# Kernel optimization log

Hardware: AMD Instinct MI355X
Metric: run time of the kernel (lower is better)

The kernel has to match this reference:

```python
import jax, jax.numpy as jnp
import numpy as np

B, L, D, NUM_ITEM, NBIN, LAYER_NUM = 1000, 50, 128, 100000, 10, 3


def _gru(x, W_ih, W_hh, b_ih, b_hh):
    # x: [B, L, Din]; torch gate order r,z,n; returns (outputs [B,L,H], h_last [B,H])
    bsz = x.shape[0]
    H = W_hh.shape[1]
    xp = jnp.einsum('bld,gd->blg', x, W_ih) + b_ih  # [B, L, 3H]

    def step(h, xp_t):
        gh = h @ W_hh.T + b_hh
        xr, xz, xn = jnp.split(xp_t, 3, axis=-1)
        hr, hz, hn = jnp.split(gh, 3, axis=-1)
        r = jax.nn.sigmoid(xr + hr)
        z = jax.nn.sigmoid(xz + hz)
        n = jnp.tanh(xn + r * hn)
        h_new = (1.0 - z) * n + z * h
        return h_new, h_new

    h0 = jnp.zeros((bsz, H), x.dtype)
    h_last, outs = jax.lax.scan(step, h0, jnp.swapaxes(xp, 0, 1))
    return jnp.swapaxes(outs, 0, 1), h_last


def _t_gcn(h, edge, edge_weight, layer_num):
    # edge-list weighted propagation; average of all layer outputs (LightGCN-style)
    src, dst = edge[0], edge[1]
    acc = h
    x = h
    for _ in range(layer_num):
        msg = x[src] * edge_weight[:, None]
        x = jax.ops.segment_sum(msg, dst, num_segments=h.shape[0])
        acc = acc + x
    return acc / (layer_num + 1)


def setup_inputs() -> dict:
    rng = np.random.default_rng(0)
    sess_len = (np.arange(B) % L) + 1
    T = int(sess_len.sum())
    seg_ids = np.repeat(np.arange(B), sess_len)
    pos_ids = np.concatenate([np.arange(L - l, L) for l in sess_len])
    n_nodes, n_edges = T, 2 * T

    key = jax.random.key(0)
    ks = jax.random.split(key, 24)
    std = 0.1

    def p(k, shape):
        return (jax.random.normal(k, shape, jnp.float32) * std)

    inp = {
        'items': jnp.asarray(rng.integers(0, NUM_ITEM, n_nodes), jnp.int32),
        'edge': jnp.asarray(rng.integers(0, n_nodes, (2, n_edges)), jnp.int32),
        'edge_weight': jax.random.uniform(ks[0], (n_edges,), jnp.float32),
        'item2idx': jnp.arange(T, dtype=jnp.int32),
        'bins': jnp.asarray(rng.integers(0, NBIN, (B, L)), jnp.int32),
        'seg_ids': jnp.asarray(seg_ids, jnp.int32),
        'pos_ids': jnp.asarray(pos_ids, jnp.int32),
        'sess_len': jnp.asarray(sess_len, jnp.int32),
        'item_emb': p(ks[1], (NUM_ITEM, D)),
        'bin_emb': p(ks[2], (NBIN, D)),
        'Wih_f': p(ks[3], (3 * D, D)), 'Whh_f': p(ks[4], (3 * D, D)),
        'bih_f': p(ks[5], (3 * D,)), 'bhh_f': p(ks[6], (3 * D,)),
        'Wih_b': p(ks[7], (3 * D, D)), 'Whh_b': p(ks[8], (3 * D, D)),
        'bih_b': p(ks[9], (3 * D,)), 'bhh_b': p(ks[10], (3 * D,)),
        'w1': p(ks[11], (1, 2 * D)),
        'w2': p(ks[12], (D, 2 * D)),
        'v3': p(ks[13], (1, D)),
        'Wih_s': p(ks[14], (3 * D, D)), 'Whh_s': p(ks[15], (3 * D, D)),
        'bih_s': p(ks[16], (3 * D,)), 'bhh_s': p(ks[17], (3 * D,)),
        'w3': p(ks[18], (1, D)), 'b3': p(ks[19], (1,)),
    }
    return inp


def reference(items, edge, edge_weight, item2idx, bins, seg_ids, pos_ids, sess_len,
              item_emb, bin_emb,
              Wih_f, Whh_f, bih_f, bhh_f, Wih_b, Whh_b, bih_b, bhh_b,
              w1, w2, v3, Wih_s, Whh_s, bih_s, bhh_s, w3, b3):
    # graph propagation over unique items, gathered back to session tokens
    h = item_emb[items]                                  # [N, D]
    h_final = _t_gcn(h, edge, edge_weight, LAYER_NUM)[item2idx]  # [T, D]

    # time-bin embedding + bidirectional GRU (dropout = identity in eval)
    e = bin_emb[bins]                                    # [B, L, D]
    out_f, _ = _gru(e, Wih_f, Whh_f, bih_f, bhh_f)
    out_b, _ = _gru(e[:, ::-1], Wih_b, Whh_b, bih_b, bhh_b)
    e_dir = jnp.concatenate([out_f, out_b[:, ::-1]], axis=-1)  # [B, L, 2D]

    b_gate = jax.nn.sigmoid(e_dir @ w1.T)                # [B, L, 1]
    e_hat_full = b_gate * e_dir[:, :, :D] + (1.0 - b_gate) * e_dir[:, :, D:]
    # take last sess_len[i] steps of each session -> ragged gather
    e_hat = e_hat_full[seg_ids, pos_ids]                 # [T, D]

    beta = jnp.tanh(jnp.concatenate([h_final, e_hat], axis=-1) @ w2.T) @ v3.T  # [T, 1]
    c = beta * h_final                                   # [T, D]

    z_long = jax.ops.segment_sum(c, seg_ids, num_segments=B)  # [B, D]

    # right-aligned pad then short GRU, keep final hidden
    c_pad = jnp.zeros((B, L, D), c.dtype).at[seg_ids, pos_ids].set(c)
    _, z_short = _gru(c_pad, Wih_s, Whh_s, bih_s, bhh_s)  # [B, D]

    f = jax.nn.sigmoid((z_long + z_short) @ w3.T + b3)   # [B, 1]
    z_final = f * z_long + (1.0 - f) * z_short
    return z_final @ item_emb.T                          # [B, NUM_ITEM]
```

## Files before the change

### kernel.cpp

```cpp
#include <hip/hip_runtime.h>
#include <hip/hip_fp16.h>

#define D    128
#define L    50
#define G3   384
#define NBIN 10
#define NNMAX 25600

#define FBM 128
#define FBN 128

typedef float f32x4 __attribute__((ext_vector_type(4)));
typedef short s16x8 __attribute__((ext_vector_type(8)));

#define MFMA_B16(a,b,c) __builtin_amdgcn_mfma_f32_16x16x32_bf16(a,b,c,0,0,0)

__device__ __forceinline__ float sigm(float x){ return 1.f/(1.f+__expf(-x)); }
__device__ __forceinline__ float tanh_fast(float x){
  float xx = fminf(fmaxf(x,-15.f),15.f);
  float e  = __expf(2.f*xx);
  return (e-1.f)/(e+1.f);
}

#define SPLIT1(x, hu, lu) { unsigned u_ = __float_as_uint(x); hu = u_ >> 16; \
  float hf_ = __uint_as_float(u_ & 0xffff0000u); float lf_ = (x) - hf_; \
  lu = __float_as_uint(lf_) >> 16; }

__device__ __forceinline__ void split8(f32x4 a, f32x4 b, s16x8& hi, s16x8& lo){
  s16x8 h, l;
#pragma unroll
  for (int i=0;i<4;++i){
    unsigned hu, lu;
    SPLIT1(a[i], hu, lu)
    h[i] = (short)hu; l[i] = (short)lu;
  }
#pragma unroll
  for (int i=0;i<4;++i){
    unsigned hu, lu;
    SPLIT1(b[i], hu, lu)
    h[4+i] = (short)hu; l[4+i] = (short)lu;
  }
  hi = h; lo = l;
}

__global__ void k_prep(const float* __restrict__ bin_emb,
                       const float* __restrict__ Wf, const float* __restrict__ bf,
                       const float* __restrict__ Wb, const float* __restrict__ bb,
                       const float* __restrict__ item_emb, const int* __restrict__ items,
                       float* __restrict__ tabf, float* __restrict__ tabb,
                       float* __restrict__ accA, float* __restrict__ xB,
                       float* __restrict__ cpad, int* __restrict__ tokmap,
                       unsigned short* __restrict__ zhi, unsigned short* __restrict__ zlo,
                       long long NG, long long BLD, int BL){
  const long long r1 = 7680, r2 = r1 + NG, r3 = r2 + BLD, r4 = r3 + BL;
  const long long ZP = 1024*128;
  const long long total = r4 + 2*ZP;
  for (long long i = (long long)blockIdx.x*256 + threadIdx.x; i < total;
       i += (long long)gridDim.x*256){
    if (i < r1){
      int id = (int)i; int dirr = id / (NBIN*G3); int rr = id % (NBIN*G3);
      int v = rr / G3, g = rr % G3;
      const float* W  = dirr ? Wb : Wf;
      const float* bi = dirr ? bb : bf;
      float a = bi[g];
      for (int d = 0; d < D; ++d) a += bin_emb[v*D+d]*W[g*D+d];
      (dirr ? tabb : tabf)[v*G3+g] = a;
    } else if (i < r2){
      long long k = i - r1;
      int nn = (int)(k>>7), d = (int)(k&127);
      float v = item_emb[(size_t)items[nn]*D + d];
      accA[k] = v; xB[k] = v;
    } else if (i < r3){
      cpad[i - r2] = 0.f;
    } else if (i < r4){
      tokmap[i - r3] = -1;
    } else {
      long long k = i - r4;
      if (k < ZP) zhi[k] = 0;
      else        zlo[k - ZP] = 0;
    }
  }
}

__global__ __launch_bounds__(1024) void k_csr1(const int* __restrict__ dst,
                                               int* __restrict__ off, int* __restrict__ cursor,
                                               int nn, int ne){
  __shared__ int degs[NNMAX];
  __shared__ int part[1024];
  int tid = threadIdx.x;
  for (int i = tid; i < nn; i += 1024) degs[i] = 0;
  __syncthreads();
  for (int e = tid; e < ne; e += 1024) atomicAdd(&degs[dst[e]], 1);
  __syncthreads();
  int chunk = (nn + 1023) >> 10;
  int c0 = tid*chunk;
  int s = 0;
  for (int k = 0; k < chunk; ++k){ int v = c0+k; if (v < nn) s += degs[v]; }
  part[tid] = s; __syncthreads();
  for (int d = 1; d < 1024; d <<= 1){
    int v = (tid >= d) ? part[tid-d] : 0;
    __syncthreads();
    part[tid] += v;
    __syncthreads();
  }
  int run = part[tid] - s;
  for (int k = 0; k < chunk; ++k){
    int v = c0+k;
    if (v < nn){ off[v] = run; cursor[v] = run; run += degs[v]; }
  }
  if (tid == 1023) off[nn] = part[1023];
}
__global__ void k_fill(const int* __restrict__ src, const int* __restrict__ dst,
                       const float* __restrict__ ew, int* __restrict__ cursor,
                       int* __restrict__ csrs, float* __restrict__ csrw, int ne){
  int e = blockIdx.x*256 + threadIdx.x;
  if (e >= ne) return;
  int p = atomicAdd(&cursor[dst[e]], 1);
  csrs[p] = src[e];
  csrw[p] = ew[e];
}
__global__ void k_gath(const float* __restrict__ x, float* __restrict__ xn,
                       float* __restrict__ acc,
                       const int* __restrict__ off, const int* __restrict__ csrs,
                       const float* __restrict__ csrw, int n){
  int i = blockIdx.x*256 + threadIdx.x;
  if (i >= n) return;
  int v = i >> 7, d = i & (D-1);
  int a = off[v], b = off[v+1];
  float s = 0.f;
  for (int k = a; k < b; ++k)
    s += x[(size_t)csrs[k]*D + d] * csrw[k];
  xn[i] = s;
  acc[i] += s;
}

__global__ __launch_bounds__(512) void k_gru_fb(
    const float* __restrict__ Whh_f, const float* __restrict__ Whh_b,
    const float* __restrict__ bhh_f, const float* __restrict__ bhh_b,
    const float* __restrict__ tabf,  const float* __restrict__ tabb,
    const int*   __restrict__ bins,  int Bn,
    float* __restrict__ outf, float* __restrict__ outbrev){
  const int dir = blockIdx.y;
  const int b0  = blockIdx.x * 16;
  const float* Whh = dir ? Whh_b : Whh_f;
  const float* bhh = dir ? bhh_b : bhh_f;
  const float* tab = dir ? tabb  : tabf;
  float* outp = dir ? outbrev : outf;

  __shared__ unsigned short hhi[2*16*128];
  __shared__ unsigned short hlo[2*16*128];
  __shared__ float xts[NBIN*G3];
  __shared__ int   binr[16][L];

  const int tid = threadIdx.x;
  const int wv = tid>>6, lane = tid&63;
  const int l15 = lane&15, lk = lane>>4;
  const int jb = wv*16;
  const int jq = jb + lk*4;

  s16x8 whi[3][4], wlo[3][4];
#pragma unroll
  for (int g3i = 0; g3i < 3; ++g3i)
#pragma unroll
    for (int ks = 0; ks < 4; ++ks){
      const f32x4* s = (const f32x4*)&Whh[(size_t)(g3i*D + jb + l15)*D + ks*32 + lk*8];
      split8(s[0], s[1], whi[g3i][ks], wlo[g3i][ks]);
    }
  f32x4 bhv[3];
#pragma unroll
  for (int g3i = 0; g3i < 3; ++g3i) bhv[g3i] = *(const f32x4*)&bhh[g3i*D + jq];

  for (int i = tid; i < NBIN*G3; i += 512) xts[i] = tab[i];
  for (int i = tid; i < 16*L; i += 512){
    int r = i / L, t = i % L;
    binr[r][t] = (b0 + r < Bn) ? bins[(b0+r)*L + (dir ? (L-1-t) : t)] : 0;
  }
  for (int i = tid; i < 2*16*128; i += 512){ hhi[i] = 0; hlo[i] = 0; }

  const int sess = l15;
  const bool sv = (b0 + sess) < Bn;
  float hreg[4] = {0.f,0.f,0.f,0.f};
  const int wbyte = sess*256 + (((jq>>3) ^ (sess&7))<<4) + ((jq&7)<<1);
  int cur = 0;
  __syncthreads();

  for (int t = 0; t < L; ++t){
    f32x4 c0a={0.f,0.f,0.f,0.f}, c1a=c0a, c2a=c0a, c0b=c0a, c1b=c0a, c2b=c0a;
    const int rb = cur*4096;
#pragma unroll
    for (int ks = 0; ks < 2; ++ks){
      int off = rb + l15*256 + ((((ks<<2)+lk) ^ (l15&7)) << 4);
      s16x8 bh8 = *(const s16x8*)((const char*)hhi + off);
      s16x8 bl8 = *(const s16x8*)((const char*)hlo + off);
      c0a = MFMA_B16(whi[0][ks], bh8, c0a); c0a = MFMA_B16(whi[0][ks], bl8, c0a); c0a = MFMA_B16(wlo[0][ks], bh8, c0a);
      c1a = MFMA_B16(whi[1][ks], bh8, c1a); c1a = MFMA_B16(whi[1][ks], bl8, c1a); c1a = MFMA_B16(wlo[1][ks], bh8, c1a);
      c2a = MFMA_B16(whi[2][ks], bh8, c2a); c2a = MFMA_B16(whi[2][ks], bl8, c2a); c2a = MFMA_B16(wlo[2][ks], bh8, c2a);
    }
#pragma unroll
    for (int ks = 2; ks < 4; ++ks){
      int off = rb + l15*256 + ((((ks<<2)+lk) ^ (l15&7)) << 4);
      s16x8 bh8 = *(const s16x8*)((const char*)hhi + off);
      s16x8 bl8 = *(const s16x8*)((const char*)hlo + off);
      c0b = MFMA_B16(whi[0][ks], bh8, c0b); c0b = MFMA_B16(whi[0][ks], bl8, c0b); c0b = MFMA_B16(wlo[0][ks], bh8, c0b);
      c1b = MFMA_B16(whi[1][ks], bh8, c1b); c1b = MFMA_B16(whi[1][ks], bl8, c1b); c1b = MFMA_B16(wlo[1][ks], bh8, c1b);
      c2b = MFMA_B16(whi[2][ks], bh8, c2b); c2b = MFMA_B16(whi[2][ks], bl8, c2b); c2b = MFMA_B16(wlo[2][ks], bh8, c2b);
    }
    f32x4 c0 = c0a + c0b, c1 = c1a + c1b, c2 = c2a + c2b;
    int bin = binr[sess][t];
    const float* xb = &xts[bin*G3];
    f32x4 xr4 = *(const f32x4*)&xb[jq];
    f32x4 xz4 = *(const f32x4*)&xb[D + jq];
    f32x4 xn4 = *(const f32x4*)&xb[2*D + jq];
    ushort4 hi4, lo4;
    f32x4 hn4;
#pragma unroll
    for (int qq = 0; qq < 4; ++qq){
      float gr = c0[qq] + bhv[0][qq];
      float gz = c1[qq] + bhv[1][qq];
      float gn = c2[qq] + bhv[2][qq];
      float rr = sigm(xr4[qq] + gr);
      float zz = sigm(xz4[qq] + gz);
      float nn = tanh_fast(xn4[qq] + rr*gn);
      float hnew = (1.f-zz)*nn + zz*hreg[qq];
      hreg[qq] = hnew;
      unsigned hu, lu; SPLIT1(hnew, hu, lu)
      ((unsigned short*)&hi4)[qq] = (unsigned short)hu;
      ((unsigned short*)&lo4)[qq] = (unsigned short)lu;
      hn4[qq] = hnew;
    }
    int wb = (cur^1)*4096 + wbyte;
    *(ushort4*)((char*)hhi + wb) = hi4;
    *(ushort4*)((char*)hlo + wb) = lo4;
    if (sv){
      float4 o = make_float4(hn4[0],hn4[1],hn4[2],hn4[3]);
      *(float4*)&outp[((size_t)(b0+sess)*L + (dir ? (L-1-t) : t))*D + jq] = o;
    }
    __syncthreads();
    cur ^= 1;
  }
}

__global__ __launch_bounds__(512) void k_beta2(
    const float* __restrict__ outf, const float* __restrict__ outbrev,
    const float* __restrict__ accA, const int* __restrict__ idxmap,
    const float* __restrict__ w1, const float* __restrict__ w2,
    const float* __restrict__ v3,
    const int* __restrict__ seg, const int* __restrict__ pos, int T,
    float* __restrict__ c_pad, int* __restrict__ tokmap){
  __shared__ unsigned short Bhi[32*256];
  __shared__ unsigned short Blo[32*256];
  __shared__ float w1s[2*D];
  __shared__ float betas[32];

  const int tid = threadIdx.x;
  const int wv = tid>>6, lane = tid&63;
  const int l15 = lane&15, lk = lane>>4;

  s16x8 w2hi[8], w2lo[8];
#pragma unroll
  for (int ks = 0; ks < 8; ++ks){
    const f32x4* s = (const f32x4*)&w2[(size_t)(wv*16 + l15)*256 + ks*32 + lk*8];
    split8(s[0], s[1], w2hi[ks], w2lo[ks]);
  }
  f32x4 v3q = *(const f32x4*)&v3[wv*16 + lk*4];
  for (int i = tid; i < 2*D; i += 512) w1s[i] = w1[i];
  __syncthreads();

  const int tok = tid >> 4;
  const int d0  = (tid & 15) * 8;
  const int sw  = (tid & 15) ^ (tok & 7);
  const int ntiles = (T + 31) >> 5;

  for (int tile = blockIdx.x; tile < ntiles; tile += gridDim.x){
    int t = tile*32 + tok;
    bool valid = (t < T);
    int sp = 0;
    f32x4 ef0 = {0,0,0,0}, ef1 = ef0, eb0 = ef0, eb1 = ef0, hf0 = ef0, hf1 = ef0;
    if (valid){
      sp = seg[t]*L + pos[t];
      const f32x4* pf = (const f32x4*)&outf[(size_t)sp*D + d0];
      const f32x4* pb = (const f32x4*)&outbrev[(size_t)sp*D + d0];
      const f32x4* ph = (const f32x4*)&accA[(size_t)idxmap[t]*D + d0];
      ef0 = pf[0]; ef1 = pf[1];
      eb0 = pb[0]; eb1 = pb[1];
      hf0 = ph[0]; hf1 = ph[1];
#pragma unroll
      for (int k=0;k<4;++k){ hf0[k]*=0.25f; hf1[k]*=0.25f; }
    }
    float p = 0.f;
#pragma unroll
    for (int k=0;k<4;++k){
      p += ef0[k]*w1s[d0+k]     + eb0[k]*w1s[D+d0+k];
      p += ef1[k]*w1s[d0+4+k]   + eb1[k]*w1s[D+d0+4+k];
    }
    p += __shfl_xor(p,1); p += __shfl_xor(p,2);
    p += __shfl_xor(p,4); p += __shfl_xor(p,8);
    float gate = sigm(p);
    f32x4 eh0, eh1;
#pragma unroll
    for (int k=0;k<4;++k){
      eh0[k] = gate*ef0[k] + (1.f-gate)*eb0[k];
      eh1[k] = gate*ef1[k] + (1.f-gate)*eb1[k];
    }
    {
      s16x8 h8, l8;
      split8(hf0, hf1, h8, l8);
      int byte = tok*512 + (sw<<4);
      *(s16x8*)((char*)Bhi + byte) = h8;
      *(s16x8*)((char*)Blo + byte) = l8;
      split8(eh0, eh1, h8, l8);
      byte = tok*512 + ((16+((tid&15)^(tok&7)))<<4);
      *(s16x8*)((char*)Bhi + byte) = h8;
      *(s16x8*)((char*)Blo + byte) = l8;
    }
    if (tid < 32) betas[tid] = 0.f;
    __syncthreads();
#pragma unroll
    for (int tt = 0; tt < 2; ++tt){
      f32x4 ca = {0.f,0.f,0.f,0.f}, cb = ca;
#pragma unroll
      for (int ks = 0; ks < 4; ++ks){
        int s_ = ((ks<<2)+lk);
        int off = (tt*16 + l15)*512 + ((s_ ^ (l15&7)) << 4);
        s16x8 bh8 = *(const s16x8*)((const char*)Bhi + off);
        s16x8 bl8 = *(const s16x8*)((const char*)Blo + off);
        ca = MFMA_B16(w2hi[ks], bh8, ca);
        ca = MFMA_B16(w2hi[ks], bl8, ca);
        ca = MFMA_B16(w2lo[ks], bh8, ca);
      }
#pragma unroll
      for (int ks = 4; ks < 8; ++ks){
        int s_ = ((ks<<2)+lk);
        int off = (tt*16 + l15)*512 + ((s_ ^ (l15&7)) << 4);
        s16x8 bh8 = *(const s16x8*)((const char*)Bhi + off);
        s16x8 bl8 = *(const s16x8*)((const char*)Blo + off);
        cb = MFMA_B16(w2hi[ks], bh8, cb);
        cb = MFMA_B16(w2hi[ks], bl8, cb);
        cb = MFMA_B16(w2lo[ks], bh8, cb);
      }
      f32x4 c = ca + cb;
      float pv = 0.f;
#pragma unroll
      for (int qq = 0; qq < 4; ++qq) pv += tanh_fast(c[qq]) * v3q[qq];
      pv += __shfl_xor(pv, 16);
      pv += __shfl_xor(pv, 32);
      if (lk == 0) atomicAdd(&betas[tt*16 + l15], pv);
    }
    __syncthreads();
    if (valid){
      float beta = betas[tok];
      f32x4 c0, c1;
#pragma unroll
      for (int k=0;k<4;++k){ c0[k] = beta*hf0[k]; c1[k] = beta*hf1[k]; }
      f32x4* pc = (f32x4*)&c_pad[(size_t)sp*D + d0];
      pc[0] = c0; pc[1] = c1;
      if ((tid & 15) == 0) tokmap[sp] = t;
    }
    __syncthreads();
  }
}

__global__ __launch_bounds__(512) void k_xps2(
    const float* __restrict__ c_pad, const int* __restrict__ seg,
    const int* __restrict__ pos, const float* __restrict__ Wih,
    const float* __restrict__ bih, int T, float* __restrict__ xps,
    float* __restrict__ zl, int Bn){
  __shared__ unsigned short Bhi[32*128];
  __shared__ unsigned short Blo[32*128];
  __shared__ float us[32*388];
  __shared__ float bihs[G3];

  const int tid = threadIdx.x;
  const int wv = tid>>6, lane = tid&63;
  const int l15 = lane&15, lk = lane>>4;
  const int gbase = wv * 48;

  for (int i = blockIdx.x*512 + tid; i < Bn*D; i += gridDim.x*512){
    int b = i >> 7, j = i & (D-1);
    float s = 0.f;
    for (int l = 0; l < L; ++l) s += c_pad[((size_t)b*L + l)*D + j];
    zl[i] = s;
  }

  s16x8 whi[3][4], wlo[3][4];
#pragma unroll
  for (int mt = 0; mt < 3; ++mt)
#pragma unroll
    for (int ks = 0; ks < 4; ++ks){
      const f32x4* s = (const f32x4*)&Wih[(size_t)(gbase + mt*16 + l15)*D + ks*32 + lk*8];
      split8(s[0], s[1], whi[mt][ks], wlo[mt][ks]);
    }
  for (int i = tid; i < G3; i += 512) bihs[i] = bih[i];
  __syncthreads();

  const int tok = tid >> 4;
  const int d0  = (tid & 15) * 8;
  const int ntiles = (T + 31) >> 5;

  for (int tile = blockIdx.x; tile < ntiles; tile += gridDim.x){
    int t = tile*32 + tok;
    bool valid = (t < T);
    f32x4 x0 = {0,0,0,0}, x1 = x0;
    if (valid){
      int sp = seg[t]*L + pos[t];
      const f32x4* pc = (const f32x4*)&c_pad[(size_t)sp*D + d0];
      x0 = pc[0]; x1 = pc[1];
    }
    {
      s16x8 h8, l8;
      split8(x0, x1, h8, l8);
      int byte = tok*256 + ((((tid&15)) ^ (tok&7))<<4);
      *(s16x8*)((char*)Bhi + byte) = h8;
      *(s16x8*)((char*)Blo + byte) = l8;
    }
    __syncthreads();
#pragma unroll
    for (int tt = 0; tt < 2; ++tt){
      f32x4 ca[3], cb[3];
#pragma unroll
      for (int mt = 0; mt < 3; ++mt){ f32x4 z = {0,0,0,0}; ca[mt] = z; cb[mt] = z; }
#pragma unroll
      for (int ks = 0; ks < 2; ++ks){
        int off = (tt*16 + l15)*256 + ((((ks<<2)+lk) ^ (l15&7)) << 4);
        s16x8 bh8 = *(const s16x8*)((const char*)Bhi + off);
        s16x8 bl8 = *(const s16x8*)((const char*)Blo + off);
        ca[0] = MFMA_B16(whi[0][ks], bh8, ca[0]); ca[0] = MFMA_B16(whi[0][ks], bl8, ca[0]); ca[0] = MFMA_B16(wlo[0][ks], bh8, ca[0]);
        ca[1] = MFMA_B16(whi[1][ks], bh8, ca[1]); ca[1] = MFMA_B16(whi[1][ks], bl8, ca[1]); ca[1] = MFMA_B16(wlo[1][ks], bh8, ca[1]);
        ca[2] = MFMA_B16(whi[2][ks], bh8, ca[2]); ca[2] = MFMA_B16(whi[2][ks], bl8, ca[2]); ca[2] = MFMA_B16(wlo[2][ks], bh8, ca[2]);
      }
#pragma unroll
      for (int ks = 2; ks < 4; ++ks){
        int off = (tt*16 + l15)*256 + ((((ks<<2)+lk) ^ (l15&7)) << 4);
        s16x8 bh8 = *(const s16x8*)((const char*)Bhi + off);
        s16x8 bl8 = *(const s16x8*)((const char*)Blo + off);
        cb[0] = MFMA_B16(whi[0][ks], bh8, cb[0]); cb[0] = MFMA_B16(whi[0][ks], bl8, cb[0]); cb[0] = MFMA_B16(wlo[0][ks], bh8, cb[0]);
        cb[1] = MFMA_B16(whi[1][ks], bh8, cb[1]); cb[1] = MFMA_B16(whi[1][ks], bl8, cb[1]); cb[1] = MFMA_B16(wlo[1][ks], bh8, cb[1]);
        cb[2] = MFMA_B16(whi[2][ks], bh8, cb[2]); cb[2] = MFMA_B16(whi[2][ks], bl8, cb[2]); cb[2] = MFMA_B16(wlo[2][ks], bh8, cb[2]);
      }
#pragma unroll
      for (int mt = 0; mt < 3; ++mt){
        f32x4 c = ca[mt] + cb[mt];
        *(f32x4*)&us[(tt*16 + l15)*388 + gbase + mt*16 + lk*4] = c;
      }
    }
    __syncthreads();
    for (int i4 = tid; i4 < 32*96; i4 += 512){
      int tk = i4 / 96, g4 = (i4 % 96) * 4;
      int tt2 = tile*32 + tk;
      if (tt2 < T){
        f32x4 u4 = *(const f32x4*)&us[tk*388 + g4];
        f32x4 b4 = *(const f32x4*)&bihs[g4];
#pragma unroll
        for (int k=0;k<4;++k) u4[k] += b4[k];
        *(f32x4*)&xps[(size_t)tt2*G3 + g4] = u4;
      }
    }
    __syncthreads();
  }
}

__global__ __launch_bounds__(512) void k_grus(
    const float* __restrict__ Whh, const float* __restrict__ bhh,
    const float* __restrict__ bih,
    const float* __restrict__ xps, const int* __restrict__ tokmap,
    const float* __restrict__ zl, const float* __restrict__ w3,
    const float* __restrict__ b3, int Bn,
    unsigned short* __restrict__ zhi, unsigned short* __restrict__ zlo,
    const float* __restrict__ emb,
    unsigned short* __restrict__ ehp, unsigned short* __restrict__ elp,
    int NI, int nslots, int nGru){
  if (blockIdx.x >= nGru){
    int nb = gridDim.x - nGru;
    for (int s = (blockIdx.x - nGru)*512 + threadIdx.x; s < nslots; s += nb*512){
      int lane = s & 63;
      int nfw  = (s>>6) & 7;
      int kk   = (s>>9) & 3;
      int ntl  = s >> 11;
      int row  = ntl*128 + (nfw>>2)*64 + (nfw&3)*16 + (lane&15);
      int d0   = kk*32 + (lane>>4)*8;
      s16x8 h8 = {0,0,0,0,0,0,0,0}, l8 = h8;
      if (row < NI){
        const f32x4* src = (const f32x4*)&emb[(size_t)row*D + d0];
        split8(src[0], src[1], h8, l8);
      }
      *(s16x8*)&ehp[(size_t)s*8] = h8;
      *(s16x8*)&elp[(size_t)s*8] = l8;
    }
    return;
  }
  const int b0 = blockIdx.x * 16;

  __shared__ unsigned short hhi[2*16*128];
  __shared__ unsigned short hlo[2*16*128];
  __shared__ int   maprow[16][L];
  __shared__ float redg[16];

  const int tid = threadIdx.x;
  const int wv = tid>>6, lane = tid&63;
  const int l15 = lane&15, lk = lane>>4;
  const int jb = wv*16;
  const int jq = jb + lk*4;

  s16x8 whi[3][4], wlo[3][4];
#pragma unroll
  for (int g3i = 0; g3i < 3; ++g3i)
#pragma unroll
    for (int ks = 0; ks < 4; ++ks){
      const f32x4* s = (const f32x4*)&Whh[(size_t)(g3i*D + jb + l15)*D + ks*32 + lk*8];
      split8(s[0], s[1], whi[g3i][ks], wlo[g3i][ks]);
    }
  f32x4 bhv[3], biv[3];
#pragma unroll
  for (int g3i = 0; g3i < 3; ++g3i){
    bhv[g3i] = *(const f32x4*)&bhh[g3i*D + jq];
    biv[g3i] = *(const f32x4*)&bih[g3i*D + jq];
  }
  for (int i = tid; i < 16*L; i += 512){
    int r = i / L, t = i % L;
    maprow[r][t] = (b0 + r < Bn) ? tokmap[(b0+r)*L + t] : -1;
  }
  for (int i = tid; i < 2*16*128; i += 512){ hhi[i] = 0; hlo[i] = 0; }

  const int sess = l15;
  const bool sv = (b0 + sess) < Bn;
  float hreg[4] = {0.f,0.f,0.f,0.f};
  const int wbyte = sess*256 + (((jq>>3) ^ (sess&7))<<4) + ((jq&7)<<1);
  int cur = 0;
  __syncthreads();

  for (int t = 0; t < L; ++t){
    int tok = maprow[sess][t];
    f32x4 xr4, xz4, xn4;
    if (tok >= 0){
      const float* xb = &xps[(size_t)tok*G3];
      xr4 = *(const f32x4*)&xb[jq];
      xz4 = *(const f32x4*)&xb[D + jq];
      xn4 = *(const f32x4*)&xb[2*D + jq];
    } else { xr4 = biv[0]; xz4 = biv[1]; xn4 = biv[2]; }
    f32x4 c0a={0.f,0.f,0.f,0.f}, c1a=c0a, c2a=c0a, c0b=c0a, c1b=c0a, c2b=c0a;
    const int rb = cur*4096;
#pragma unroll
    for (int ks = 0; ks < 2; ++ks){
      int off = rb + l15*256 + ((((ks<<2)+lk) ^ (l15&7)) << 4);
      s16x8 bh8 = *(const s16x8*)((const char*)hhi + off);
      s16x8 bl8 = *(const s16x8*)((const char*)hlo + off);
      c0a = MFMA_B16(whi[0][ks], bh8, c0a); c0a = MFMA_B16(whi[0][ks], bl8, c0a); c0a = MFMA_B16(wlo[0][ks], bh8, c0a);
      c1a = MFMA_B16(whi[1][ks], bh8, c1a); c1a = MFMA_B16(whi[1][ks], bl8, c1a); c1a = MFMA_B16(wlo[1][ks], bh8, c1a);
      c2a = MFMA_B16(whi[2][ks], bh8, c2a); c2a = MFMA_B16(whi[2][ks], bl8, c2a); c2a = MFMA_B16(wlo[2][ks], bh8, c2a);
    }
#pragma unroll
    for (int ks = 2; ks < 4; ++ks){
      int off = rb + l15*256 + ((((ks<<2)+lk) ^ (l15&7)) << 4);
      s16x8 bh8 = *(const s16x8*)((const char*)hhi + off);
      s16x8 bl8 = *(const s16x8*)((const char*)hlo + off);
      c0b = MFMA_B16(whi[0][ks], bh8, c0b); c0b = MFMA_B16(whi[0][ks], bl8, c0b); c0b = MFMA_B16(wlo[0][ks], bh8, c0b);
      c1b = MFMA_B16(whi[1][ks], bh8, c1b); c1b = MFMA_B16(whi[1][ks], bl8, c1b); c1b = MFMA_B16(wlo[1][ks], bh8, c1b);
      c2b = MFMA_B16(whi[2][ks], bh8, c2b); c2b = MFMA_B16(whi[2][ks], bl8, c2b); c2b = MFMA_B16(wlo[2][ks], bh8, c2b);
    }
    f32x4 c0 = c0a + c0b, c1 = c1a + c1b, c2 = c2a + c2b;
    ushort4 hi4, lo4;
#pragma unroll
    for (int qq = 0; qq < 4; ++qq){
      float gr = c0[qq] + bhv[0][qq];
      float gz = c1[qq] + bhv[1][qq];
      float gn = c2[qq] + bhv[2][qq];
      float rr = sigm(xr4[qq] + gr);
      float zz = sigm(xz4[qq] + gz);
      float nn = tanh_fast(xn4[qq] + rr*gn);
      float hnew = (1.f-zz)*nn + zz*hreg[qq];
      hreg[qq] = hnew;
      unsigned hu, lu; SPLIT1(hnew, hu, lu)
      ((unsigned short*)&hi4)[qq] = (unsigned short)hu;
      ((unsigned short*)&lo4)[qq] = (unsigned short)lu;
    }
    int wb = (cur^1)*4096 + wbyte;
    *(ushort4*)((char*)hhi + wb) = hi4;
    *(ushort4*)((char*)hlo + wb) = lo4;
    __syncthreads();
    cur ^= 1;
  }

  if (tid < 16) redg[tid] = 0.f;
  __syncthreads();
  f32x4 zl4 = {0.f,0.f,0.f,0.f};
  if (sv) zl4 = *(const f32x4*)&zl[(size_t)(b0+sess)*D + jq];
  f32x4 w34 = *(const f32x4*)&w3[jq];
  float part = 0.f;
#pragma unroll
  for (int qq = 0; qq < 4; ++qq) part += (zl4[qq] + hreg[qq]) * w34[qq];
  if (sv) atomicAdd(&redg[sess], part);
  __syncthreads();
  if (sv){
    float f = sigm(redg[sess] + b3[0]);
    ushort4 h4, l4;
#pragma unroll
    for (int qq = 0; qq < 4; ++qq){
      float zv = f*zl4[qq] + (1.f-f)*hreg[qq];
      unsigned hu, lu; SPLIT1(zv, hu, lu)
      ((unsigned short*)&h4)[qq] = (unsigned short)hu;
      ((unsigned short*)&l4)[qq] = (unsigned short)lu;
    }
    int row = b0 + sess;
    int mtile = row >> 7, r128 = row & 127;
    int wmr = r128 >> 6, mfr = (r128 >> 4) & 3, l15r = r128 & 15;
    int kkr = jq >> 5, lkr = (jq & 31) >> 3, e0 = jq & 7;
    int laner = lkr*16 + l15r;
    size_t slot = ((size_t)(((mtile*4 + kkr)*2 + wmr)*4 + mfr))*64 + laner;
    *(ushort4*)&zhi[slot*8 + e0] = h4;
    *(ushort4*)&zlo[slot*8 + e0] = l4;
  }
}

__global__ __launch_bounds__(256, 3) void k_fmm(
    const unsigned short* __restrict__ zhi, const unsigned short* __restrict__ zlo,
    const unsigned short* __restrict__ ehp, const unsigned short* __restrict__ elp,
    float* __restrict__ out, int NI, int Bsz){
  __shared__ float fs[64*136];

  int nwg = gridDim.x;
  int hw  = blockIdx.x;
  int q8 = nwg >> 3, r8 = nwg & 7;
  int xcd = hw & 7, idx = hw >> 3;
  int logical = (xcd < r8 ? xcd*(q8+1) : r8*(q8+1) + (xcd-r8)*q8) + idx;
  int ntile = logical >> 3;
  int mtile = logical & 7;
  int m0 = mtile*FBM;
  int n0 = ntile*FBN;

  const int t    = threadIdx.x;
  const int lane = t & 63;
  const int wid  = t >> 6;
  const int wm   = wid >> 1, wn = wid & 1;
  const int l15  = lane & 15, lk = lane >> 4;

  f32x4 acc[4][4];
#pragma unroll
  for (int i = 0; i < 4; ++i)
#pragma unroll
    for (int jj = 0; jj < 4; ++jj){ f32x4 z4 = {0.f,0.f,0.f,0.f}; acc[i][jj] = z4; }

#pragma unroll
  for (int kk = 0; kk < 4; ++kk){
    s16x8 ah[4], al[4], bh8[4], bl8[4];
#pragma unroll
    for (int mf = 0; mf < 4; ++mf){
      size_t slot = ((size_t)(((mtile*4 + kk)*2 + wm)*4 + mf))*64 + lane;
      ah[mf] = *(const s16x8*)&zhi[slot*8];
      al[mf] = *(const s16x8*)&zlo[slot*8];
    }
#pragma unroll
    for (int nf = 0; nf < 4; ++nf){
      size_t slot = ((size_t)((ntile*4 + kk)*8 + wn*4 + nf))*64 + lane;
      bh8[nf] = *(const s16x8*)&ehp[slot*8];
      bl8[nf] = *(const s16x8*)&elp[slot*8];
    }
#pragma unroll
    for (int mf = 0; mf < 4; ++mf)
#pragma unroll
      for (int nf = 0; nf < 4; ++nf){
        acc[mf][nf] = MFMA_B16(ah[mf], bh8[nf], acc[mf][nf]);
        acc[mf][nf] = MFMA_B16(ah[mf], bl8[nf], acc[mf][nf]);
        acc[mf][nf] = MFMA_B16(al[mf], bh8[nf], acc[mf][nf]);
      }
  }

#pragma unroll
  for (int p = 0; p < 2; ++p){
    __syncthreads();
    if (wm == p){
#pragma unroll
      for (int mf = 0; mf < 4; ++mf)
#pragma unroll
        for (int nf = 0; nf < 4; ++nf)
#pragma unroll
          for (int qq = 0; qq < 4; ++qq)
            fs[(mf*16 + lk*4 + qq)*136 + wn*64 + nf*16 + l15] = acc[mf][nf][qq];
    }
    __syncthreads();
#pragma unroll
    for (int it = 0; it < 8; ++it){
      int row = (t>>5) + it*8;
      int col = (t&31)*4;
      f32x4 v = *(const f32x4*)&fs[row*136 + col];
      int gr = m0 + p*64 + row;
      if (gr < Bsz && n0 + col < NI)
        __builtin_nontemporal_store(v, (f32x4*)&out[(size_t)gr*NI + n0 + col]);
    }
  }
}

extern "C" void kernel_launch(void* const* d_in, const int* in_sizes, int n_in,
                              void* d_out, int out_size, void* d_ws, size_t ws_size,
                              hipStream_t stream){
  const int*   items    = (const int*)d_in[0];
  const int*   edge     = (const int*)d_in[1];
  const float* ew       = (const float*)d_in[2];
  const int*   item2idx = (const int*)d_in[3];
  const int*   bins     = (const int*)d_in[4];
  const int*   seg      = (const int*)d_in[5];
  const int*   pos      = (const int*)d_in[6];
  const float* item_emb = (const float*)d_in[8];
  const float* bin_emb  = (const float*)d_in[9];
  const float* Wih_f = (const float*)d_in[10];
  const float* Whh_f = (const float*)d_in[11];
  const float* bih_f = (const float*)d_in[12];
  const float* bhh_f = (const float*)d_in[13];
  const float* Wih_b = (const float*)d_in[14];
  const float* Whh_b = (const float*)d_in[15];
  const float* bih_b = (const float*)d_in[16];
  const float* bhh_b = (const float*)d_in[17];
  const float* w1    = (const float*)d_in[18];
  const float* w2    = (const float*)d_in[19];
  const float* v3    = (const float*)d_in[20];
  const float* Wih_s = (const float*)d_in[21];
  const float* Whh_s = (const float*)d_in[22];
  const float* bih_s = (const float*)d_in[23];
  const float* bhh_s = (const float*)d_in[24];
  const float* w3    = (const float*)d_in[25];
  const float* b3    = (const float*)d_in[26];
  float* out = (float*)d_out;

  const int NN = in_sizes[0];
  const int NE = in_sizes[2];
  const int T  = in_sizes[3];
  const int B  = in_sizes[7];
  const int NI = in_sizes[8] / D;

  const size_t NG  = (size_t)NN * D;
  const size_t BLD = (size_t)B * L * D;
  const int ntilesN = (NI + FBN - 1)/FBN;
  const int nslots  = ntilesN * 2048;

  float* ws   = (float*)d_ws;
  float* accA = ws;
  float* xB   = ws + NG;
  float* xC   = ws + 2*NG;
  float* xps  = ws;
  float* outf = ws + 3*NG;
  float* outb = outf + BLD;
  float* cpad = outb + BLD;
  int*   tokmap = (int*)(cpad + BLD);
  float* tabf = (float*)(tokmap + (size_t)B*L);
  float* tabb = tabf + NBIN*G3;
  float* zl   = tabb + NBIN*G3;
  unsigned short* zhi = (unsigned short*)(zl + (size_t)B*D);
  unsigned short* zlo = zhi + 1024*128;
  int* off    = (int*)(zlo + 1024*128);
  int* cursor = off + NN + 1;
  int* csrs   = cursor + NN;
  float* csrw = (float*)(csrs + NE);
  unsigned short* ehp = (unsigned short*)(csrw + NE);
  unsigned short* elp = ehp + (size_t)nslots*8;

  hipLaunchKernelGGL(k_prep, dim3(2048), dim3(256), 0, stream,
                     bin_emb, Wih_f, bih_f, Wih_b, bih_b, item_emb, items,
                     tabf, tabb, accA, xB, cpad, tokmap, zhi, zlo,
                     (long long)NG, (long long)BLD, B*L);
  hipLaunchKernelGGL(k_csr1, dim3(1), dim3(1024), 0, stream, edge+NE, off, cursor, NN, NE);
  hipLaunchKernelGGL(k_fill, dim3((NE+255)/256), dim3(256), 0, stream,
                     edge, edge+NE, ew, cursor, csrs, csrw, NE);
  const int ggrid = (int)((NG + 255)/256);
  hipLaunchKernelGGL(k_gath, dim3(ggrid), dim3(256), 0, stream, xB, xC, accA, off, csrs, csrw, (int)NG);
  hipLaunchKernelGGL(k_gath, dim3(ggrid), dim3(256), 0, stream, xC, xB, accA, off, csrs, csrw, (int)NG);
  hipLaunchKernelGGL(k_gath, dim3(ggrid), dim3(256), 0, stream, xB, xC, accA, off, csrs, csrw, (int)NG);
  hipLaunchKernelGGL(k_gru_fb, dim3((B+15)/16, 2), dim3(512), 0, stream,
                     Whh_f, Whh_b, bhh_f, bhh_b, tabf, tabb, bins, B, outf, outb);
  hipLaunchKernelGGL(k_beta2, dim3(256), dim3(512), 0, stream,
                     outf, outb, accA, item2idx, w1, w2, v3, seg, pos, T, cpad, tokmap);
  hipLaunchKernelGGL(k_xps2, dim3(256), dim3(512), 0, stream,
                     cpad, seg, pos, Wih_s, bih_s, T, xps, zl, B);
  {
    int nGru = (B + 15)/16;
    hipLaunchKernelGGL(k_grus, dim3(256), dim3(512), 0, stream,
                       Whh_s, bhh_s, bih_s, xps, tokmap, zl, w3, b3, B, zhi, zlo,
                       item_emb, ehp, elp, NI, nslots, nGru);
  }
  {
    int mtiles = (B + FBM - 1)/FBM;
    hipLaunchKernelGGL(k_fmm, dim3(mtiles*ntilesN), dim3(256), 0, stream,
                       zhi, zlo, ehp, elp, out, NI, B);
  }
}
```

Measured before the change: 446.3 us.

## Fuse CSR fill into degree kernel and attention with short-GRU input projection

```diff
diff --git a/kernel.cpp b/kernel.cpp
--- a/kernel.cpp
+++ b/kernel.cpp
@@ -82,8 +82,11 @@
   }
 }
 
-__global__ __launch_bounds__(1024) void k_csr1(const int* __restrict__ dst,
-                                               int* __restrict__ off, int* __restrict__ cursor,
+__global__ __launch_bounds__(1024) void k_csr1(const int* __restrict__ src,
+                                               const int* __restrict__ dst,
+                                               const float* __restrict__ ew,
+                                               int* __restrict__ off,
+                                               int* __restrict__ csrs, float* __restrict__ csrw,
                                                int nn, int ne){
   __shared__ int degs[NNMAX];
   __shared__ int part[1024];
@@ -106,19 +109,22 @@
   int run = part[tid] - s;
   for (int k = 0; k < chunk; ++k){
     int v = c0+k;
-    if (v < nn){ off[v] = run; cursor[v] = run; run += degs[v]; }
+    if (v < nn){
+      off[v] = run;
+      int dv = degs[v];
+      degs[v] = run;
+      run += dv;
+    }
   }
   if (tid == 1023) off[nn] = part[1023];
-}
-__global__ void k_fill(const int* __restrict__ src, const int* __restrict__ dst,
-                       const float* __restrict__ ew, int* __restrict__ cursor,
-                       int* __restrict__ csrs, float* __restrict__ csrw, int ne){
-  int e = blockIdx.x*256 + threadIdx.x;
-  if (e >= ne) return;
-  int p = atomicAdd(&cursor[dst[e]], 1);
-  csrs[p] = src[e];
-  csrw[p] = ew[e];
-}
+  __syncthreads();
+  for (int e = tid; e < ne; e += 1024){
+    int p = atomicAdd(&degs[dst[e]], 1);
+    csrs[p] = src[e];
+    csrw[p] = ew[e];
+  }
+}
+
 __global__ void k_gath(const float* __restrict__ x, float* __restrict__ xn,
                        float* __restrict__ acc,
                        const int* __restrict__ off, const int* __restrict__ csrs,
@@ -240,21 +246,26 @@
   }
 }
 
-__global__ __launch_bounds__(512) void k_beta2(
+__global__ __launch_bounds__(512) void k_attn(
     const float* __restrict__ outf, const float* __restrict__ outbrev,
     const float* __restrict__ accA, const int* __restrict__ idxmap,
     const float* __restrict__ w1, const float* __restrict__ w2,
     const float* __restrict__ v3,
+    const float* __restrict__ Wih, const float* __restrict__ bih,
     const int* __restrict__ seg, const int* __restrict__ pos, int T,
-    float* __restrict__ c_pad, int* __restrict__ tokmap){
+    float* __restrict__ c_pad, int* __restrict__ tokmap,
+    float* __restrict__ xps){
   __shared__ unsigned short Bhi[32*256];
   __shared__ unsigned short Blo[32*256];
+  __shared__ float us[32*388];
   __shared__ float w1s[2*D];
+  __shared__ float bihs[G3];
   __shared__ float betas[32];
 
   const int tid = threadIdx.x;
   const int wv = tid>>6, lane = tid&63;
   const int l15 = lane&15, lk = lane>>4;
+  const int gbase = wv * 48;
 
   s16x8 w2hi[8], w2lo[8];
 #pragma unroll
@@ -263,7 +274,16 @@
     split8(s[0], s[1], w2hi[ks], w2lo[ks]);
   }
   f32x4 v3q = *(const f32x4*)&v3[wv*16 + lk*4];
+  s16x8 whi[3][4], wlo[3][4];
+#pragma unroll
+  for (int mt = 0; mt < 3; ++mt)
+#pragma unroll
+    for (int ks = 0; ks < 4; ++ks){
+      const f32x4* s = (const f32x4*)&Wih[(size_t)(gbase + mt*16 + l15)*D + ks*32 + lk*8];
+      split8(s[0], s[1], whi[mt][ks], wlo[mt][ks]);
+    }
   for (int i = tid; i < 2*D; i += 512) w1s[i] = w1[i];
+  for (int i = tid; i < G3;  i += 512) bihs[i] = bih[i];
   __syncthreads();
 
   const int tok = tid >> 4;
@@ -309,7 +329,7 @@
       *(s16x8*)((char*)Bhi + byte) = h8;
       *(s16x8*)((char*)Blo + byte) = l8;
       split8(eh0, eh1, h8, l8);
-      byte = tok*512 + ((16+((tid&15)^(tok&7)))<<4);
+      byte = tok*512 + ((16+sw)<<4);
       *(s16x8*)((char*)Bhi + byte) = h8;
       *(s16x8*)((char*)Blo + byte) = l8;
     }
@@ -347,69 +367,19 @@
       if (lk == 0) atomicAdd(&betas[tt*16 + l15], pv);
     }
     __syncthreads();
+    f32x4 c0v = {0,0,0,0}, c1v = c0v;
     if (valid){
       float beta = betas[tok];
-      f32x4 c0, c1;
-#pragma unroll
-      for (int k=0;k<4;++k){ c0[k] = beta*hf0[k]; c1[k] = beta*hf1[k]; }
+#pragma unroll
+      for (int k=0;k<4;++k){ c0v[k] = beta*hf0[k]; c1v[k] = beta*hf1[k]; }
       f32x4* pc = (f32x4*)&c_pad[(size_t)sp*D + d0];
-      pc[0] = c0; pc[1] = c1;
+      pc[0] = c0v; pc[1] = c1v;
       if ((tid & 15) == 0) tokmap[sp] = t;
-    }
-    __syncthreads();
-  }
-}
-
-__global__ __launch_bounds__(512) void k_xps2(
-    const float* __restrict__ c_pad, const int* __restrict__ seg,
-    const int* __restrict__ pos, const float* __restrict__ Wih,
-    const float* __restrict__ bih, int T, float* __restrict__ xps,
-    float* __restrict__ zl, int Bn){
-  __shared__ unsigned short Bhi[32*128];
-  __shared__ unsigned short Blo[32*128];
-  __shared__ float us[32*388];
-  __shared__ float bihs[G3];
-
-  const int tid = threadIdx.x;
-  const int wv = tid>>6, lane = tid&63;
-  const int l15 = lane&15, lk = lane>>4;
-  const int gbase = wv * 48;
-
-  for (int i = blockIdx.x*512 + tid; i < Bn*D; i += gridDim.x*512){
-    int b = i >> 7, j = i & (D-1);
-    float s = 0.f;
-    for (int l = 0; l < L; ++l) s += c_pad[((size_t)b*L + l)*D + j];
-    zl[i] = s;
-  }
-
-  s16x8 whi[3][4], wlo[3][4];
-#pragma unroll
-  for (int mt = 0; mt < 3; ++mt)
-#pragma unroll
-    for (int ks = 0; ks < 4; ++ks){
-      const f32x4* s = (const f32x4*)&Wih[(size_t)(gbase + mt*16 + l15)*D + ks*32 + lk*8];
-      split8(s[0], s[1], whi[mt][ks], wlo[mt][ks]);
-    }
-  for (int i = tid; i < G3; i += 512) bihs[i] = bih[i];
-  __syncthreads();
-
-  const int tok = tid >> 4;
-  const int d0  = (tid & 15) * 8;
-  const int ntiles = (T + 31) >> 5;
-
-  for (int tile = blockIdx.x; tile < ntiles; tile += gridDim.x){
-    int t = tile*32 + tok;
-    bool valid = (t < T);
-    f32x4 x0 = {0,0,0,0}, x1 = x0;
-    if (valid){
-      int sp = seg[t]*L + pos[t];
-      const f32x4* pc = (const f32x4*)&c_pad[(size_t)sp*D + d0];
-      x0 = pc[0]; x1 = pc[1];
     }
     {
       s16x8 h8, l8;
-      split8(x0, x1, h8, l8);
-      int byte = tok*256 + ((((tid&15)) ^ (tok&7))<<4);
+      split8(c0v, c1v, h8, l8);
+      int byte = tok*256 + (sw<<4);
       *(s16x8*)((char*)Bhi + byte) = h8;
       *(s16x8*)((char*)Blo + byte) = l8;
     }
@@ -463,7 +433,7 @@
     const float* __restrict__ Whh, const float* __restrict__ bhh,
     const float* __restrict__ bih,
     const float* __restrict__ xps, const int* __restrict__ tokmap,
-    const float* __restrict__ zl, const float* __restrict__ w3,
+    const float* __restrict__ c_pad, const float* __restrict__ w3,
     const float* __restrict__ b3, int Bn,
     unsigned short* __restrict__ zhi, unsigned short* __restrict__ zlo,
     const float* __restrict__ emb,
@@ -583,7 +553,11 @@
   if (tid < 16) redg[tid] = 0.f;
   __syncthreads();
   f32x4 zl4 = {0.f,0.f,0.f,0.f};
-  if (sv) zl4 = *(const f32x4*)&zl[(size_t)(b0+sess)*D + jq];
+  if (sv){
+    const size_t rowbase = (size_t)(b0+sess)*L;
+    for (int l = 0; l < L; ++l)
+      zl4 += *(const f32x4*)&c_pad[(rowbase + l)*D + jq];
+  }
   f32x4 w34 = *(const f32x4*)&w3[jq];
   float part = 0.f;
 #pragma unroll
@@ -735,44 +709,40 @@
   float* accA = ws;
   float* xB   = ws + NG;
   float* xC   = ws + 2*NG;
-  float* xps  = ws;
   float* outf = ws + 3*NG;
   float* outb = outf + BLD;
   float* cpad = outb + BLD;
   int*   tokmap = (int*)(cpad + BLD);
   float* tabf = (float*)(tokmap + (size_t)B*L);
   float* tabb = tabf + NBIN*G3;
-  float* zl   = tabb + NBIN*G3;
-  unsigned short* zhi = (unsigned short*)(zl + (size_t)B*D);
+  unsigned short* zhi = (unsigned short*)(tabb + NBIN*G3);
   unsigned short* zlo = zhi + 1024*128;
   int* off    = (int*)(zlo + 1024*128);
-  int* cursor = off + NN + 1;
-  int* csrs   = cursor + NN;
+  int* csrs   = off + NN + 1;
   float* csrw = (float*)(csrs + NE);
   unsigned short* ehp = (unsigned short*)(csrw + NE);
   unsigned short* elp = ehp + (size_t)nslots*8;
+  float* xps  = (float*)(elp + (size_t)nslots*8);
 
   hipLaunchKernelGGL(k_prep, dim3(2048), dim3(256), 0, stream,
                      bin_emb, Wih_f, bih_f, Wih_b, bih_b, item_emb, items,
                      tabf, tabb, accA, xB, cpad, tokmap, zhi, zlo,
                      (long long)NG, (long long)BLD, B*L);
-  hipLaunchKernelGGL(k_csr1, dim3(1), dim3(1024), 0, stream, edge+NE, off, cursor, NN, NE);
-  hipLaunchKernelGGL(k_fill, dim3((NE+255)/256), dim3(256), 0, stream,
-                     edge, edge+NE, ew, cursor, csrs, csrw, NE);
+  hipLaunchKernelGGL(k_csr1, dim3(1), dim3(1024), 0, stream,
+                     edge, edge+NE, ew, off, csrs, csrw, NN, NE);
   const int ggrid = (int)((NG + 255)/256);
   hipLaunchKernelGGL(k_gath, dim3(ggrid), dim3(256), 0, stream, xB, xC, accA, off, csrs, csrw, (int)NG);
   hipLaunchKernelGGL(k_gath, dim3(ggrid), dim3(256), 0, stream, xC, xB, accA, off, csrs, csrw, (int)NG);
   hipLaunchKernelGGL(k_gath, dim3(ggrid), dim3(256), 0, stream, xB, xC, accA, off, csrs, csrw, (int)NG);
   hipLaunchKernelGGL(k_gru_fb, dim3((B+15)/16, 2), dim3(512), 0, stream,
                      Whh_f, Whh_b, bhh_f, bhh_b, tabf, tabb, bins, B, outf, outb);
-  hipLaunchKernelGGL(k_beta2, dim3(256), dim3(512), 0, stream,
-                     outf, outb, accA, item2idx, w1, w2, v3, seg, pos, T, cpad, tokmap);
-  hipLaunchKernelGGL(k_xps2, dim3(256), dim3(512), 0, stream,
-                     cpad, seg, pos, Wih_s, bih_s, T, xps, zl, B);
+  hipLaunchKernelGGL(k_attn, dim3(256), dim3(512), 0, stream,
+                     outf, outb, accA, item2idx, w1, w2, v3, Wih_s, bih_s,
+                     seg, pos, T, cpad, tokmap, xps);
   {
     int nGru = (B + 15)/16;
     hipLaunchKernelGGL(k_grus, dim3(256), dim3(512), 0, stream,
-                       Whh_s, bhh_s, bih_s, xps, tokmap, zl, w3, b3, B, zhi, zlo,
+                       Whh_s, bhh_s, bih_s, xps, tokmap, cpad, w3, b3, B, zhi, zlo,
                        item_emb, ehp, elp, NI, nslots, nGru);
   }
   {
```

Result: slower. 546.8 us (+22.5%).

## Fuse CSR fill into single-block build and fold last GCN layer into beta kernel

Applied to the files above, without the earlier changes.

```diff
diff --git a/kernel.cpp b/kernel.cpp
--- a/kernel.cpp
+++ b/kernel.cpp
@@ -82,8 +82,11 @@
   }
 }
 
-__global__ __launch_bounds__(1024) void k_csr1(const int* __restrict__ dst,
-                                               int* __restrict__ off, int* __restrict__ cursor,
+__global__ __launch_bounds__(1024) void k_csrf(const int* __restrict__ src,
+                                               const int* __restrict__ dst,
+                                               const float* __restrict__ ew,
+                                               int* __restrict__ off,
+                                               int* __restrict__ csrs, float* __restrict__ csrw,
                                                int nn, int ne){
   __shared__ int degs[NNMAX];
   __shared__ int part[1024];
@@ -106,19 +109,22 @@
   int run = part[tid] - s;
   for (int k = 0; k < chunk; ++k){
     int v = c0+k;
-    if (v < nn){ off[v] = run; cursor[v] = run; run += degs[v]; }
+    if (v < nn){
+      off[v] = run;
+      int dv = degs[v];
+      degs[v] = run;
+      run += dv;
+    }
   }
   if (tid == 1023) off[nn] = part[1023];
-}
-__global__ void k_fill(const int* __restrict__ src, const int* __restrict__ dst,
-                       const float* __restrict__ ew, int* __restrict__ cursor,
-                       int* __restrict__ csrs, float* __restrict__ csrw, int ne){
-  int e = blockIdx.x*256 + threadIdx.x;
-  if (e >= ne) return;
-  int p = atomicAdd(&cursor[dst[e]], 1);
-  csrs[p] = src[e];
-  csrw[p] = ew[e];
-}
+  __syncthreads();
+  for (int e = tid; e < ne; e += 1024){
+    int p = atomicAdd(&degs[dst[e]], 1);
+    csrs[p] = src[e];
+    csrw[p] = ew[e];
+  }
+}
+
 __global__ void k_gath(const float* __restrict__ x, float* __restrict__ xn,
                        float* __restrict__ acc,
                        const int* __restrict__ off, const int* __restrict__ csrs,
@@ -243,6 +249,9 @@
 __global__ __launch_bounds__(512) void k_beta2(
     const float* __restrict__ outf, const float* __restrict__ outbrev,
     const float* __restrict__ accA, const int* __restrict__ idxmap,
+    const float* __restrict__ xl2,
+    const int* __restrict__ off, const int* __restrict__ csrs,
+    const float* __restrict__ csrw,
     const float* __restrict__ w1, const float* __restrict__ w2,
     const float* __restrict__ v3,
     const int* __restrict__ seg, const int* __restrict__ pos, int T,
@@ -280,12 +289,19 @@
       sp = seg[t]*L + pos[t];
       const f32x4* pf = (const f32x4*)&outf[(size_t)sp*D + d0];
       const f32x4* pb = (const f32x4*)&outbrev[(size_t)sp*D + d0];
-      const f32x4* ph = (const f32x4*)&accA[(size_t)idxmap[t]*D + d0];
       ef0 = pf[0]; ef1 = pf[1];
       eb0 = pb[0]; eb1 = pb[1];
-      hf0 = ph[0]; hf1 = ph[1];
-#pragma unroll
-      for (int k=0;k<4;++k){ hf0[k]*=0.25f; hf1[k]*=0.25f; }
+      int nv = idxmap[t];
+      const f32x4* ph = (const f32x4*)&accA[(size_t)nv*D + d0];
+      f32x4 ha0 = ph[0], ha1 = ph[1];
+      int a0 = off[nv], a1 = off[nv+1];
+      for (int k = a0; k < a1; ++k){
+        float ww = csrw[k];
+        const f32x4* px = (const f32x4*)&xl2[(size_t)csrs[k]*D + d0];
+        ha0 += px[0]*ww; ha1 += px[1]*ww;
+      }
+#pragma unroll
+      for (int k=0;k<4;++k){ hf0[k] = ha0[k]*0.25f; hf1[k] = ha1[k]*0.25f; }
     }
     float p = 0.f;
 #pragma unroll
@@ -309,7 +325,7 @@
       *(s16x8*)((char*)Bhi + byte) = h8;
       *(s16x8*)((char*)Blo + byte) = l8;
       split8(eh0, eh1, h8, l8);
-      byte = tok*512 + ((16+((tid&15)^(tok&7)))<<4);
+      byte = tok*512 + ((16+sw)<<4);
       *(s16x8*)((char*)Bhi + byte) = h8;
       *(s16x8*)((char*)Blo + byte) = l8;
     }
@@ -321,9 +337,9 @@
 #pragma unroll
       for (int ks = 0; ks < 4; ++ks){
         int s_ = ((ks<<2)+lk);
-        int off = (tt*16 + l15)*512 + ((s_ ^ (l15&7)) << 4);
-        s16x8 bh8 = *(const s16x8*)((const char*)Bhi + off);
-        s16x8 bl8 = *(const s16x8*)((const char*)Blo + off);
+        int off_ = (tt*16 + l15)*512 + ((s_ ^ (l15&7)) << 4);
+        s16x8 bh8 = *(const s16x8*)((const char*)Bhi + off_);
+        s16x8 bl8 = *(const s16x8*)((const char*)Blo + off_);
         ca = MFMA_B16(w2hi[ks], bh8, ca);
         ca = MFMA_B16(w2hi[ks], bl8, ca);
         ca = MFMA_B16(w2lo[ks], bh8, ca);
@@ -331,9 +347,9 @@
 #pragma unroll
       for (int ks = 4; ks < 8; ++ks){
         int s_ = ((ks<<2)+lk);
-        int off = (tt*16 + l15)*512 + ((s_ ^ (l15&7)) << 4);
-        s16x8 bh8 = *(const s16x8*)((const char*)Bhi + off);
-        s16x8 bl8 = *(const s16x8*)((const char*)Blo + off);
+        int off_ = (tt*16 + l15)*512 + ((s_ ^ (l15&7)) << 4);
+        s16x8 bh8 = *(const s16x8*)((const char*)Bhi + off_);
+        s16x8 bl8 = *(const s16x8*)((const char*)Blo + off_);
         cb = MFMA_B16(w2hi[ks], bh8, cb);
         cb = MFMA_B16(w2hi[ks], bl8, cb);
         cb = MFMA_B16(w2lo[ks], bh8, cb);
@@ -746,8 +762,7 @@
   unsigned short* zhi = (unsigned short*)(zl + (size_t)B*D);
   unsigned short* zlo = zhi + 1024*128;
   int* off    = (int*)(zlo + 1024*128);
-  int* cursor = off + NN + 1;
-  int* csrs   = cursor + NN;
+  int* csrs   = off + NN + 1;
   float* csrw = (float*)(csrs + NE);
   unsigned short* ehp = (unsigned short*)(csrw + NE);
   unsigned short* elp = ehp + (size_t)nslots*8;
@@ -756,17 +771,16 @@
                      bin_emb, Wih_f, bih_f, Wih_b, bih_b, item_emb, items,
                      tabf, tabb, accA, xB, cpad, tokmap, zhi, zlo,
                      (long long)NG, (long long)BLD, B*L);
-  hipLaunchKernelGGL(k_csr1, dim3(1), dim3(1024), 0, stream, edge+NE, off, cursor, NN, NE);
-  hipLaunchKernelGGL(k_fill, dim3((NE+255)/256), dim3(256), 0, stream,
-                     edge, edge+NE, ew, cursor, csrs, csrw, NE);
+  hipLaunchKernelGGL(k_csrf, dim3(1), dim3(1024), 0, stream,
+                     edge, edge+NE, ew, off, csrs, csrw, NN, NE);
   const int ggrid = (int)((NG + 255)/256);
   hipLaunchKernelGGL(k_gath, dim3(ggrid), dim3(256), 0, stream, xB, xC, accA, off, csrs, csrw, (int)NG);
   hipLaunchKernelGGL(k_gath, dim3(ggrid), dim3(256), 0, stream, xC, xB, accA, off, csrs, csrw, (int)NG);
-  hipLaunchKernelGGL(k_gath, dim3(ggrid), dim3(256), 0, stream, xB, xC, accA, off, csrs, csrw, (int)NG);
   hipLaunchKernelGGL(k_gru_fb, dim3((B+15)/16, 2), dim3(512), 0, stream,
                      Whh_f, Whh_b, bhh_f, bhh_b, tabf, tabb, bins, B, outf, outb);
   hipLaunchKernelGGL(k_beta2, dim3(256), dim3(512), 0, stream,
-                     outf, outb, accA, item2idx, w1, w2, v3, seg, pos, T, cpad, tokmap);
+                     outf, outb, accA, item2idx, xB, off, csrs, csrw,
+                     w1, w2, v3, seg, pos, T, cpad, tokmap);
   hipLaunchKernelGGL(k_xps2, dim3(256), dim3(512), 0, stream,
                      cpad, seg, pos, Wih_s, bih_s, T, xps, zl, B);
   {
```

New measurement: 507.3 us. 13.6% more time.
